# Kernel optimization log

Measured on AMD Instinct MI355X. Metric: run time of the kernel, lower is better.

## Reference

```python
import jax, jax.numpy as jnp
import numpy as np

B, T, D_MODEL, N_HEADS, D_FF = 2, 2048, 512, 8, 2048
D_HEAD = D_MODEL // N_HEADS
EPS_LN = 1e-5
DEN_MIN = 1e-6


def setup_inputs() -> dict:
    key = jax.random.key(0)
    ks = jax.random.split(key, 12)
    def lin_w(k, din, dout):
        return jax.random.normal(k, (din, dout), jnp.float32) / np.sqrt(din).astype(np.float32)
    return {
        "x": jax.random.normal(ks[0], (B, T, D_MODEL), jnp.float32),
        "ln1_g": jnp.ones((D_MODEL,), jnp.float32),
        "ln1_b": jnp.zeros((D_MODEL,), jnp.float32),
        "Wq": lin_w(ks[1], D_MODEL, D_MODEL), "bq": jnp.zeros((D_MODEL,), jnp.float32),
        "Wk": lin_w(ks[2], D_MODEL, D_MODEL), "bk": jnp.zeros((D_MODEL,), jnp.float32),
        "Wv": lin_w(ks[3], D_MODEL, D_MODEL), "bv": jnp.zeros((D_MODEL,), jnp.float32),
        "Wo": lin_w(ks[4], D_MODEL, D_MODEL), "bo": jnp.zeros((D_MODEL,), jnp.float32),
        "ln2_g": jnp.ones((D_MODEL,), jnp.float32),
        "ln2_b": jnp.zeros((D_MODEL,), jnp.float32),
        "W1": lin_w(ks[5], D_MODEL, D_FF), "b1": jnp.zeros((D_FF,), jnp.float32),
        "W2": lin_w(ks[6], D_FF, D_MODEL), "b2": jnp.zeros((D_MODEL,), jnp.float32),
    }


def layer_norm(x, g, b):
    mu = jnp.mean(x, axis=-1, keepdims=True)
    var = jnp.var(x, axis=-1, keepdims=True)
    return (x - mu) * jax.lax.rsqrt(var + EPS_LN) * g + b


def causal_linear_attention(Q, K, V):
    # Q,K,V: (B,H,T,D); feature map already applied to Q,K.
    # Running summary S_t = cumsum_j phi(K_j) outer V_j, shape (B,H,T,D,D)
    KV = jnp.cumsum(K[..., :, None] * V[..., None, :], axis=2)
    z = jnp.cumsum(K, axis=2)                                   # (B,H,T,D)
    num = jnp.einsum('bhtd,bhtdm->bhtm', Q, KV)                 # (B,H,T,D)
    den = jnp.maximum(jnp.einsum('bhtd,bhtd->bht', Q, z), DEN_MIN)[..., None]
    return num / den


def reference(x, ln1_g, ln1_b, Wq, bq, Wk, bk, Wv, bv, Wo, bo,
              ln2_g, ln2_b, W1, b1, W2, b2):
    Bx, Tx, _ = x.shape
    # --- sublayer 1: pre-norm causal linear attention + residual ---
    h = layer_norm(x, ln1_g, ln1_b)
    def heads(y):  # (B,T,D_MODEL) -> (B,H,T,D_HEAD)
        return y.reshape(Bx, Tx, N_HEADS, D_HEAD).transpose(0, 2, 1, 3)
    Q = jax.nn.elu(heads(h @ Wq + bq)) + 1.0
    K = jax.nn.elu(heads(h @ Wk + bk)) + 1.0
    V = heads(h @ Wv + bv)
    attn = causal_linear_attention(Q, K, V)                     # (B,H,T,D)
    attn = attn.transpose(0, 2, 1, 3).reshape(Bx, Tx, D_MODEL)
    x = x + (attn @ Wo + bo)
    # --- sublayer 2: pre-norm FFN + residual (dropout=0, eval mode) ---
    h2 = layer_norm(x, ln2_g, ln2_b)
    ffn = jax.nn.relu(h2 @ W1 + b1) @ W2 + b2
    return x + ffn
```

## Files before the change

### kernel.cpp

```cpp
#include <hip/hip_runtime.h>
#include <hip/hip_bf16.h>
#include <cstdint>

#define T_SEQ   2048
#define DM      512
#define NH      8
#define DH      64
#define BATCH   2
#define MROWS   4096
#define DFF     2048
#define CHUNK   64
#define NCHUNK  32
#define BHN     16
#define ST_STRIDE 4160

typedef __attribute__((ext_vector_type(8))) short bf16x8;
typedef __attribute__((ext_vector_type(4))) float f32x4;
typedef __hip_bfloat16 bf16;

__device__ __forceinline__ void g2lds16(const bf16* g, bf16* l) {
    __builtin_amdgcn_global_load_lds(
        (const __attribute__((address_space(1))) unsigned int*)g,
        (__attribute__((address_space(3))) unsigned int*)l, 16, 0, 0);
}

template<bool INIT>
__global__ __launch_bounds__(128) void ln_kernel(
    const float* __restrict__ x, const float* __restrict__ g,
    const float* __restrict__ b, bf16* __restrict__ y,
    const float* __restrict__ b2, float* __restrict__ oinit)
{
    int row = blockIdx.x;
    int t = threadIdx.x;
    const float4* xr = (const float4*)(x + (size_t)row * DM);
    float4 v = xr[t];
    float s  = v.x + v.y + v.z + v.w;
    float s2 = v.x*v.x + v.y*v.y + v.z*v.z + v.w*v.w;
#pragma unroll
    for (int off = 32; off > 0; off >>= 1) {
        s  += __shfl_down(s,  off);
        s2 += __shfl_down(s2, off);
    }
    __shared__ float sh[4];
    if ((t & 63) == 0) { sh[(t >> 6) * 2] = s; sh[(t >> 6) * 2 + 1] = s2; }
    __syncthreads();
    s  = sh[0] + sh[2];
    s2 = sh[1] + sh[3];
    float mu  = s * (1.0f / DM);
    float var = s2 * (1.0f / DM) - mu * mu;
    float rs  = rsqrtf(var + 1e-5f);
    float4 gg = ((const float4*)g)[t];
    float4 bb = ((const float4*)b)[t];
    union { short4 s4; bf16 h[4]; } u;
    u.h[0] = __float2bfloat16((v.x - mu) * rs * gg.x + bb.x);
    u.h[1] = __float2bfloat16((v.y - mu) * rs * gg.y + bb.y);
    u.h[2] = __float2bfloat16((v.z - mu) * rs * gg.z + bb.z);
    u.h[3] = __float2bfloat16((v.w - mu) * rs * gg.w + bb.w);
    *(short4*)(y + (size_t)row * DM + t * 4) = u.s4;
    if (INIT) {
        float4 b2v = ((const float4*)b2)[t];
        float4 ov = make_float4(v.x + b2v.x, v.y + b2v.y, v.z + b2v.z, v.w + b2v.w);
        ((float4*)(oinit + (size_t)row * DM))[t] = ov;
    }
}

__global__ __launch_bounds__(256) void wcvt_all(
    const float* __restrict__ Wq, const float* __restrict__ Wk,
    const float* __restrict__ Wv, const float* __restrict__ Wo,
    const float* __restrict__ W1, const float* __restrict__ W2,
    bf16* __restrict__ QKVWT, bf16* __restrict__ WoT,
    bf16* __restrict__ W1T, bf16* __restrict__ W2T)
{
    __shared__ float tile[64][65];
    int bid = blockIdx.x;
    const float* src; bf16* dst; int K, N, txi, tyi;
    if (bid < 256) {
        int m = bid >> 6, t = bid & 63;
        src = m == 0 ? Wq : m == 1 ? Wk : m == 2 ? Wv : Wo;
        dst = m == 0 ? QKVWT : m == 1 ? QKVWT + 512*512
            : m == 2 ? QKVWT + 1024*512 : WoT;
        K = 512; N = 512; txi = t & 7; tyi = t >> 3;
    } else if (bid < 512) {
        int t = bid - 256;
        src = W1; dst = W1T; K = 512; N = 2048; txi = t & 31; tyi = t >> 5;
    } else {
        int t = bid - 512;
        src = W2; dst = W2T; K = 2048; N = 512; txi = t & 7; tyi = t >> 3;
    }
    int k0 = tyi * 64, n0 = txi * 64;
    int tid = threadIdx.x;
    int tr = tid >> 4, tc = (tid & 15) * 4;
#pragma unroll
    for (int i = 0; i < 4; i++) {
        float4 v = *(const float4*)(src + (size_t)(k0 + tr + i*16) * N + n0 + tc);
        tile[tr + i*16][tc+0] = v.x; tile[tr + i*16][tc+1] = v.y;
        tile[tr + i*16][tc+2] = v.z; tile[tr + i*16][tc+3] = v.w;
    }
    __syncthreads();
#pragma unroll
    for (int i = 0; i < 4; i++) {
        int n = tr + i*16;
        union { short4 s4; bf16 h[4]; } u;
#pragma unroll
        for (int j = 0; j < 4; j++) u.h[j] = __float2bfloat16(tile[tc+j][n]);
        *(short4*)(dst + (size_t)(n0 + n) * K + k0 + tc) = u.s4;
    }
}

template<int BM, int BN, int WM, int WN, int MODE>
__global__ __launch_bounds__(WM*WN*64) void mfma_gemm(
    const bf16* __restrict__ A, const bf16* __restrict__ Bt,
    const float* __restrict__ bias0, const float* __restrict__ bias1,
    const float* __restrict__ bias2, const float* __restrict__ res,
    float* __restrict__ outF,
    float* __restrict__ outQ, float* __restrict__ outK, float* __restrict__ outV,
    bf16* __restrict__ outB, int M, int N, int K)
{
    constexpr int BK = 64;
    constexpr int WAVES = WM * WN;
    constexpr int WTM = BM / WM, WTN = BN / WN;
    constexpr int FM = WTM / 16, FN = WTN / 16;
    constexpr int IA = BM / 8 / WAVES, IB = BN / 8 / WAVES;
    __shared__ bf16 As[BM * BK];
    __shared__ bf16 Bs[BN * BK];
    const int tid = threadIdx.x;
    const int w = tid >> 6, lane = tid & 63;
    const int wr = w / WN, wc = w % WN;
    const int bm0 = blockIdx.y * BM, bn0 = blockIdx.x * BN;
    const int srow = lane >> 3;
    const int scol = (lane & 7) * 8;

    int kbeg = 0, kend = K;
    if (MODE == 3) { int half = K >> 1; kbeg = blockIdx.z * half; kend = kbeg + half; }

    f32x4 acc[FM][FN];
#pragma unroll
    for (int m = 0; m < FM; m++)
#pragma unroll
        for (int n = 0; n < FN; n++) acc[m][n] = (f32x4){0.f,0.f,0.f,0.f};

    for (int k0 = kbeg; k0 < kend; k0 += BK) {
#pragma unroll
        for (int i = 0; i < IA; i++) {
            int c = i*WAVES + w;
            g2lds16(A + (size_t)(bm0 + c*8 + srow) * K + k0 + scol, &As[c*512]);
        }
#pragma unroll
        for (int i = 0; i < IB; i++) {
            int c = i*WAVES + w;
            g2lds16(Bt + (size_t)(bn0 + c*8 + srow) * K + k0 + scol, &Bs[c*512]);
        }
        __syncthreads();
#pragma unroll
        for (int kk = 0; kk < 2; kk++) {
            bf16x8 af[FM], bfr[FN];
#pragma unroll
            for (int m = 0; m < FM; m++)
                af[m] = *(const bf16x8*)&As[(wr*WTM + m*16 + (lane&15))*BK + kk*32 + (lane>>4)*8];
#pragma unroll
            for (int n = 0; n < FN; n++)
                bfr[n] = *(const bf16x8*)&Bs[(wc*WTN + n*16 + (lane&15))*BK + kk*32 + (lane>>4)*8];
#pragma unroll
            for (int m = 0; m < FM; m++)
#pragma unroll
                for (int n = 0; n < FN; n++)
                    acc[m][n] = __builtin_amdgcn_mfma_f32_16x16x32_bf16(af[m], bfr[n], acc[m][n], 0, 0, 0);
        }
        __syncthreads();
    }

    const int lr = (lane >> 4) * 4;
    const int lc = lane & 15;
#pragma unroll
    for (int m = 0; m < FM; m++) {
#pragma unroll
        for (int n = 0; n < FN; n++) {
            int col = bn0 + wc*WTN + n*16 + lc;
#pragma unroll
            for (int j = 0; j < 4; j++) {
                int r = bm0 + wr*WTM + m*16 + lr + j;
                float v = acc[m][n][j];
                if (MODE == 0) {
                    int which = col >> 9;
                    int cc = col & 511;
                    float bv_ = which == 0 ? bias0[cc] : which == 1 ? bias1[cc] : bias2[cc];
                    v += bv_;
                    if (which < 2) v = v > 0.f ? v + 1.f : __expf(v);
                    int hh = cc >> 6, dd = cc & 63;
                    int bb = r >> 11, tt = r & 2047;
                    float* dst = which == 0 ? outQ : which == 1 ? outK : outV;
                    dst[((((size_t)(bb*NH + hh)) * T_SEQ + tt) << 6) + dd] = v;
                } else if (MODE == 1) {
                    v += bias0[col] + res[(size_t)r * N + col];
                    outF[(size_t)r * N + col] = v;
                } else if (MODE == 2) {
                    v += bias0[col];
                    v = fmaxf(v, 0.f);
                    outB[(size_t)r * N + col] = __float2bfloat16(v);
                } else {
                    unsafeAtomicAdd(&outF[(size_t)r * N + col], v);
                }
            }
        }
    }
}

__global__ __launch_bounds__(256) void attn_chunk_sum(
    const float* __restrict__ Kb, const float* __restrict__ Vb,
    float* __restrict__ St)
{
    int blk = blockIdx.x;
    const float* Kp = Kb + (size_t)blk * (CHUNK * DH);
    const float* Vp = Vb + (size_t)blk * (CHUNK * DH);
    float* Sp = St + (size_t)blk * ST_STRIDE;
    __shared__ float Ks[64][64];
    __shared__ float Vs[64][64];
    int tid = threadIdx.x;
#pragma unroll
    for (int i = 0; i < 4; i++) {
        ((float4*)Ks)[tid + i*256] = ((const float4*)Kp)[tid + i*256];
        ((float4*)Vs)[tid + i*256] = ((const float4*)Vp)[tid + i*256];
    }
    __syncthreads();
    int r  = tid >> 2;
    int c0 = (tid & 3) * 16;
    float s[16];
#pragma unroll
    for (int i = 0; i < 16; i++) s[i] = 0.0f;
    for (int t = 0; t < 64; t++) {
        float kv = Ks[t][r];
        const float4* vr = (const float4*)&Vs[t][c0];
        float4 v0 = vr[0], v1 = vr[1], v2 = vr[2], v3 = vr[3];
        s[0]+=kv*v0.x; s[1]+=kv*v0.y; s[2]+=kv*v0.z; s[3]+=kv*v0.w;
        s[4]+=kv*v1.x; s[5]+=kv*v1.y; s[6]+=kv*v1.z; s[7]+=kv*v1.w;
        s[8]+=kv*v2.x; s[9]+=kv*v2.y; s[10]+=kv*v2.z; s[11]+=kv*v2.w;
        s[12]+=kv*v3.x; s[13]+=kv*v3.y; s[14]+=kv*v3.z; s[15]+=kv*v3.w;
    }
#pragma unroll
    for (int i = 0; i < 4; i++) {
        float4 ov = make_float4(s[i*4+0], s[i*4+1], s[i*4+2], s[i*4+3]);
        *(float4*)(Sp + (size_t)r*64 + c0 + i*4) = ov;
    }
    if (tid < 64) {
        float z = 0.0f;
        for (int t = 0; t < 64; t++) z += Ks[t][tid];
        Sp[4096 + tid] = z;
    }
}

__global__ __launch_bounds__(64) void attn_scan(float* __restrict__ St)
{
    int f4 = blockIdx.x * 64 + threadIdx.x;
    if (f4 >= ST_STRIDE / 4) return;
    int bh = blockIdx.y;
    float4* base = (float4*)(St + (size_t)bh * NCHUNK * ST_STRIDE) + f4;
    float4 run = make_float4(0.f, 0.f, 0.f, 0.f);
#pragma unroll 4
    for (int ch = 0; ch < NCHUNK; ch++) {
        float4* p = base + (size_t)ch * (ST_STRIDE / 4);
        float4 t = *p;
        *p = run;
        run.x += t.x; run.y += t.y; run.z += t.z; run.w += t.w;
    }
}

__global__ __launch_bounds__(256) void attn_out_k(
    const float* __restrict__ Qb, const float* __restrict__ Kb,
    const float* __restrict__ Vb, const float* __restrict__ St,
    bf16* __restrict__ attnb)
{
    int blk = blockIdx.x;
    int bh = blk >> 5, ch = blk & 31;
    int b = bh >> 3, h = bh & 7;
    const float* Qp = Qb + (size_t)blk * 4096;
    const float* Kp = Kb + (size_t)blk * 4096;
    const float* Vp = Vb + (size_t)blk * 4096;
    const float* Sp = St + (size_t)blk * ST_STRIDE;
    __shared__ float Qs[64][68];
    __shared__ float Kt[64][68];
    __shared__ float Vs[64][68];
    __shared__ float Ss[64][68];
    __shared__ float Amat[64][65];
    __shared__ float zs[64];
    int tid = threadIdx.x;
#pragma unroll
    for (int i = 0; i < 4; i++) {
        int fi = tid + i*256;
        int t  = fi >> 4;
        int d4 = (fi & 15) * 4;
        float4 q = ((const float4*)Qp)[fi];
        float4 k = ((const float4*)Kp)[fi];
        float4 v = ((const float4*)Vp)[fi];
        float4 s = ((const float4*)Sp)[fi];
        *(float4*)&Qs[t][d4] = q;
        *(float4*)&Vs[t][d4] = v;
        *(float4*)&Ss[t][d4] = s;
        Kt[d4+0][t] = k.x; Kt[d4+1][t] = k.y; Kt[d4+2][t] = k.z; Kt[d4+3][t] = k.w;
    }
    if (tid < 64) zs[tid] = Sp[4096 + tid];
    __syncthreads();
    int r  = tid >> 2;
    int c0 = (tid & 3) * 16;
    float a[16];
#pragma unroll
    for (int i = 0; i < 16; i++) a[i] = 0.0f;
    for (int d = 0; d < 64; d++) {
        float q = Qs[r][d];
        const float4* kr = (const float4*)&Kt[d][c0];
        float4 k0 = kr[0], k1 = kr[1], k2 = kr[2], k3 = kr[3];
        a[0]+=q*k0.x; a[1]+=q*k0.y; a[2]+=q*k0.z; a[3]+=q*k0.w;
        a[4]+=q*k1.x; a[5]+=q*k1.y; a[6]+=q*k1.z; a[7]+=q*k1.w;
        a[8]+=q*k2.x; a[9]+=q*k2.y; a[10]+=q*k2.z; a[11]+=q*k2.w;
        a[12]+=q*k3.x; a[13]+=q*k3.y; a[14]+=q*k3.z; a[15]+=q*k3.w;
    }
#pragma unroll
    for (int i = 0; i < 16; i++) Amat[r][c0+i] = a[i];
    __syncthreads();
    float den = 0.0f;
    for (int d = 0; d < 64; d++) den += Qs[r][d] * zs[d];
    for (int j = 0; j <= r; j++) den += Amat[r][j];
    den = fmaxf(den, 1e-6f);
    float num[16];
#pragma unroll
    for (int i = 0; i < 16; i++) num[i] = 0.0f;
    for (int d = 0; d < 64; d++) {
        float q = Qs[r][d];
        const float4* sv = (const float4*)&Ss[d][c0];
        float4 s0 = sv[0], s1 = sv[1], s2 = sv[2], s3 = sv[3];
        num[0]+=q*s0.x; num[1]+=q*s0.y; num[2]+=q*s0.z; num[3]+=q*s0.w;
        num[4]+=q*s1.x; num[5]+=q*s1.y; num[6]+=q*s1.z; num[7]+=q*s1.w;
        num[8]+=q*s2.x; num[9]+=q*s2.y; num[10]+=q*s2.z; num[11]+=q*s2.w;
        num[12]+=q*s3.x; num[13]+=q*s3.y; num[14]+=q*s3.z; num[15]+=q*s3.w;
    }
    for (int j = 0; j <= r; j++) {
        float aj = Amat[r][j];
        const float4* vv = (const float4*)&Vs[j][c0];
        float4 v0 = vv[0], v1 = vv[1], v2 = vv[2], v3 = vv[3];
        num[0]+=aj*v0.x; num[1]+=aj*v0.y; num[2]+=aj*v0.z; num[3]+=aj*v0.w;
        num[4]+=aj*v1.x; num[5]+=aj*v1.y; num[6]+=aj*v1.z; num[7]+=aj*v1.w;
        num[8]+=aj*v2.x; num[9]+=aj*v2.y; num[10]+=aj*v2.z; num[11]+=aj*v2.w;
        num[12]+=aj*v3.x; num[13]+=aj*v3.y; num[14]+=aj*v3.z; num[15]+=aj*v3.w;
    }
    float inv = 1.0f / den;
    union { short4 s4[4]; bf16 hh[16]; } u;
#pragma unroll
    for (int i = 0; i < 16; i++) u.hh[i] = __float2bfloat16(num[i] * inv);
    short4* op = (short4*)(attnb + ((size_t)b * T_SEQ + ch*64 + r) * DM + h*64 + c0);
#pragma unroll
    for (int i = 0; i < 4; i++) op[i] = u.s4[i];
}

extern "C" void kernel_launch(void* const* d_in, const int* in_sizes, int n_in,
                              void* d_out, int out_size, void* d_ws, size_t ws_size,
                              hipStream_t stream)
{
    (void)in_sizes; (void)n_in; (void)out_size; (void)ws_size;
    const float* x     = (const float*)d_in[0];
    const float* ln1_g = (const float*)d_in[1];
    const float* ln1_b = (const float*)d_in[2];
    const float* Wq = (const float*)d_in[3];
    const float* bq = (const float*)d_in[4];
    const float* Wk = (const float*)d_in[5];
    const float* bk = (const float*)d_in[6];
    const float* Wv = (const float*)d_in[7];
    const float* bv = (const float*)d_in[8];
    const float* Wo = (const float*)d_in[9];
    const float* bo = (const float*)d_in[10];
    const float* ln2_g = (const float*)d_in[11];
    const float* ln2_b = (const float*)d_in[12];
    const float* W1 = (const float*)d_in[13];
    const float* b1 = (const float*)d_in[14];
    const float* W2 = (const float*)d_in[15];
    const float* b2 = (const float*)d_in[16];
    float* out = (float*)d_out;
    char* base = (char*)d_ws;

    bf16*  h_bf  = (bf16*)(base + 0);
    bf16*  h2_bf = (bf16*)(base + 4194304);
    bf16*  attnb = (bf16*)(base + 8388608);
    bf16*  QKVWT = (bf16*)(base + 12582912);
    bf16*  WoT   = (bf16*)(base + 14155776);
    bf16*  W1T   = (bf16*)(base + 14680064);
    bf16*  W2T   = (bf16*)(base + 16777216);
    float* Qb    = (float*)(base + 18874368);
    float* Kb    = (float*)(base + 27262976);
    float* Vb    = (float*)(base + 35651584);
    float* St    = (float*)(base + 44040192);
    float* X2    = (float*)(base + 52559872);
    bf16*  FF    = (bf16*)(base + 60948480);

    wcvt_all<<<768, 256, 0, stream>>>(Wq, Wk, Wv, Wo, W1, W2,
                                      QKVWT, WoT, W1T, W2T);

    ln_kernel<false><<<MROWS, 128, 0, stream>>>(x, ln1_g, ln1_b, h_bf, nullptr, nullptr);

    mfma_gemm<128,128,4,2,0><<<dim3(12, 32), 512, 0, stream>>>(
        h_bf, QKVWT, bq, bk, bv, nullptr, nullptr, Qb, Kb, Vb, nullptr,
        MROWS, 1536, 512);

    attn_chunk_sum<<<BHN*NCHUNK, 256, 0, stream>>>(Kb, Vb, St);
    attn_scan<<<dim3(17, BHN), 64, 0, stream>>>(St);
    attn_out_k<<<BHN*NCHUNK, 256, 0, stream>>>(Qb, Kb, Vb, St, attnb);

    mfma_gemm<64,64,2,2,1><<<dim3(8, 64), 256, 0, stream>>>(
        attnb, WoT, bo, nullptr, nullptr, x, X2, nullptr, nullptr, nullptr, nullptr,
        MROWS, 512, 512);

    ln_kernel<true><<<MROWS, 128, 0, stream>>>(X2, ln2_g, ln2_b, h2_bf, b2, out);

    mfma_gemm<128,128,4,2,2><<<dim3(16, 32), 512, 0, stream>>>(
        h2_bf, W1T, b1, nullptr, nullptr, nullptr, nullptr, nullptr, nullptr, nullptr, FF,
        MROWS, DFF, 512);

    mfma_gemm<128,64,2,2,3><<<dim3(8, 32, 2), 256, 0, stream>>>(
        FF, W2T, nullptr, nullptr, nullptr, nullptr, out, nullptr, nullptr, nullptr, nullptr,
        MROWS, 512, 2048);
}
```

Before: 228.7 us.

## Store Q/K/V intermediates in bf16, bf16 attention matrix, XCD-aware GEMM block swizzle

The QKV GEMM epilogue now writes Q, K and V as bf16 instead of fp32, and the chunk-sum and chunk-output attention kernels load and widen bf16x8 vectors. This halves the intermediate traffic to and from global memory. The in-chunk attention score matrix is kept in bf16 in shared memory. An XCD-aware block-index swizzle is added to all GEMMs to improve L2 locality across chiplets. The cost is reduced precision in the attention path and extra index arithmetic.

New measurement: 212.6 us. 1.08x faster.

```diff
diff --git a/kernel.cpp b/kernel.cpp
--- a/kernel.cpp
+++ b/kernel.cpp
@@ -22,6 +22,21 @@
     __builtin_amdgcn_global_load_lds(
         (const __attribute__((address_space(1))) unsigned int*)g,
         (__attribute__((address_space(3))) unsigned int*)l, 16, 0, 0);
+}
+
+__device__ __forceinline__ float b2f(short s) {
+    union { unsigned u; float f; } x;
+    x.u = ((unsigned)(unsigned short)s) << 16;
+    return x.f;
+}
+
+__device__ __forceinline__ void xcd_swizzle(int gx, int gy, int& bx, int& by) {
+    int lin = by * gx + bx;
+    int nwg = gx * gy;
+    int q = nwg >> 3, r = nwg & 7;
+    int xcd = lin & 7, loc = lin >> 3;
+    int swz = (xcd < r ? xcd * (q + 1) : r * (q + 1) + (xcd - r) * q) + loc;
+    bx = swz % gx; by = swz / gx;
 }
 
 template<bool INIT>
@@ -113,7 +128,7 @@
     const float* __restrict__ bias0, const float* __restrict__ bias1,
     const float* __restrict__ bias2, const float* __restrict__ res,
     float* __restrict__ outF,
-    float* __restrict__ outQ, float* __restrict__ outK, float* __restrict__ outV,
+    bf16* __restrict__ outQ, bf16* __restrict__ outK, bf16* __restrict__ outV,
     bf16* __restrict__ outB, int M, int N, int K)
 {
     constexpr int BK = 64;
@@ -126,7 +141,9 @@
     const int tid = threadIdx.x;
     const int w = tid >> 6, lane = tid & 63;
     const int wr = w / WN, wc = w % WN;
-    const int bm0 = blockIdx.y * BM, bn0 = blockIdx.x * BN;
+    int bx = blockIdx.x, by = blockIdx.y;
+    xcd_swizzle(gridDim.x, gridDim.y, bx, by);
+    const int bm0 = by * BM, bn0 = bx * BN;
     const int srow = lane >> 3;
     const int scol = (lane & 7) * 8;
 
@@ -188,8 +205,8 @@
                     if (which < 2) v = v > 0.f ? v + 1.f : __expf(v);
                     int hh = cc >> 6, dd = cc & 63;
                     int bb = r >> 11, tt = r & 2047;
-                    float* dst = which == 0 ? outQ : which == 1 ? outK : outV;
-                    dst[((((size_t)(bb*NH + hh)) * T_SEQ + tt) << 6) + dd] = v;
+                    bf16* dst = which == 0 ? outQ : which == 1 ? outK : outV;
+                    dst[((((size_t)(bb*NH + hh)) * T_SEQ + tt) << 6) + dd] = __float2bfloat16(v);
                 } else if (MODE == 1) {
                     v += bias0[col] + res[(size_t)r * N + col];
                     outF[(size_t)r * N + col] = v;
@@ -206,20 +223,27 @@
 }
 
 __global__ __launch_bounds__(256) void attn_chunk_sum(
-    const float* __restrict__ Kb, const float* __restrict__ Vb,
+    const bf16* __restrict__ Kb, const bf16* __restrict__ Vb,
     float* __restrict__ St)
 {
     int blk = blockIdx.x;
-    const float* Kp = Kb + (size_t)blk * (CHUNK * DH);
-    const float* Vp = Vb + (size_t)blk * (CHUNK * DH);
+    const bf16* Kp = Kb + (size_t)blk * (CHUNK * DH);
+    const bf16* Vp = Vb + (size_t)blk * (CHUNK * DH);
     float* Sp = St + (size_t)blk * ST_STRIDE;
     __shared__ float Ks[64][64];
     __shared__ float Vs[64][64];
     int tid = threadIdx.x;
 #pragma unroll
-    for (int i = 0; i < 4; i++) {
-        ((float4*)Ks)[tid + i*256] = ((const float4*)Kp)[tid + i*256];
-        ((float4*)Vs)[tid + i*256] = ((const float4*)Vp)[tid + i*256];
+    for (int i = 0; i < 2; i++) {
+        int idx = tid + i*256;
+        int t = idx >> 3, d8 = (idx & 7) * 8;
+        bf16x8 k8 = ((const bf16x8*)Kp)[idx];
+        bf16x8 v8 = ((const bf16x8*)Vp)[idx];
+#pragma unroll
+        for (int j = 0; j < 8; j++) {
+            Ks[t][d8+j] = b2f(k8[j]);
+            Vs[t][d8+j] = b2f(v8[j]);
+        }
     }
     __syncthreads();
     int r  = tid >> 2;
@@ -265,37 +289,45 @@
 }
 
 __global__ __launch_bounds__(256) void attn_out_k(
-    const float* __restrict__ Qb, const float* __restrict__ Kb,
-    const float* __restrict__ Vb, const float* __restrict__ St,
+    const bf16* __restrict__ Qb, const bf16* __restrict__ Kb,
+    const bf16* __restrict__ Vb, const float* __restrict__ St,
     bf16* __restrict__ attnb)
 {
     int blk = blockIdx.x;
     int bh = blk >> 5, ch = blk & 31;
     int b = bh >> 3, h = bh & 7;
-    const float* Qp = Qb + (size_t)blk * 4096;
-    const float* Kp = Kb + (size_t)blk * 4096;
-    const float* Vp = Vb + (size_t)blk * 4096;
+    const bf16*  Qp = Qb + (size_t)blk * 4096;
+    const bf16*  Kp = Kb + (size_t)blk * 4096;
+    const bf16*  Vp = Vb + (size_t)blk * 4096;
     const float* Sp = St + (size_t)blk * ST_STRIDE;
     __shared__ float Qs[64][68];
     __shared__ float Kt[64][68];
     __shared__ float Vs[64][68];
     __shared__ float Ss[64][68];
-    __shared__ float Amat[64][65];
+    __shared__ bf16  Amat[64][72];
     __shared__ float zs[64];
     int tid = threadIdx.x;
+#pragma unroll
+    for (int i = 0; i < 2; i++) {
+        int idx = tid + i*256;
+        int t = idx >> 3, d8 = (idx & 7) * 8;
+        bf16x8 q8 = ((const bf16x8*)Qp)[idx];
+        bf16x8 k8 = ((const bf16x8*)Kp)[idx];
+        bf16x8 v8 = ((const bf16x8*)Vp)[idx];
+#pragma unroll
+        for (int j = 0; j < 8; j++) {
+            Qs[t][d8+j] = b2f(q8[j]);
+            Vs[t][d8+j] = b2f(v8[j]);
+            Kt[d8+j][t] = b2f(k8[j]);
+        }
+    }
 #pragma unroll
     for (int i = 0; i < 4; i++) {
         int fi = tid + i*256;
         int t  = fi >> 4;
         int d4 = (fi & 15) * 4;
-        float4 q = ((const float4*)Qp)[fi];
-        float4 k = ((const float4*)Kp)[fi];
-        float4 v = ((const float4*)Vp)[fi];
         float4 s = ((const float4*)Sp)[fi];
-        *(float4*)&Qs[t][d4] = q;
-        *(float4*)&Vs[t][d4] = v;
         *(float4*)&Ss[t][d4] = s;
-        Kt[d4+0][t] = k.x; Kt[d4+1][t] = k.y; Kt[d4+2][t] = k.z; Kt[d4+3][t] = k.w;
     }
     if (tid < 64) zs[tid] = Sp[4096 + tid];
     __syncthreads();
@@ -313,12 +345,15 @@
         a[8]+=q*k2.x; a[9]+=q*k2.y; a[10]+=q*k2.z; a[11]+=q*k2.w;
         a[12]+=q*k3.x; a[13]+=q*k3.y; a[14]+=q*k3.z; a[15]+=q*k3.w;
     }
-#pragma unroll
-    for (int i = 0; i < 16; i++) Amat[r][c0+i] = a[i];
+    union { bf16x8 v8[2]; bf16 hh[16]; } ua;
+#pragma unroll
+    for (int i = 0; i < 16; i++) ua.hh[i] = __float2bfloat16(a[i]);
+    *(bf16x8*)&Amat[r][c0]   = ua.v8[0];
+    *(bf16x8*)&Amat[r][c0+8] = ua.v8[1];
     __syncthreads();
     float den = 0.0f;
     for (int d = 0; d < 64; d++) den += Qs[r][d] * zs[d];
-    for (int j = 0; j <= r; j++) den += Amat[r][j];
+    for (int j = 0; j <= r; j++) den += b2f(*(const short*)&Amat[r][j]);
     den = fmaxf(den, 1e-6f);
     float num[16];
 #pragma unroll
@@ -333,7 +368,7 @@
         num[12]+=q*s3.x; num[13]+=q*s3.y; num[14]+=q*s3.z; num[15]+=q*s3.w;
     }
     for (int j = 0; j <= r; j++) {
-        float aj = Amat[r][j];
+        float aj = b2f(*(const short*)&Amat[r][j]);
         const float4* vv = (const float4*)&Vs[j][c0];
         float4 v0 = vv[0], v1 = vv[1], v2 = vv[2], v3 = vv[3];
         num[0]+=aj*v0.x; num[1]+=aj*v0.y; num[2]+=aj*v0.z; num[3]+=aj*v0.w;
@@ -374,20 +409,21 @@
     const float* b2 = (const float*)d_in[16];
     float* out = (float*)d_out;
     char* base = (char*)d_ws;
+    const size_t MB = 1048576;
 
     bf16*  h_bf  = (bf16*)(base + 0);
-    bf16*  h2_bf = (bf16*)(base + 4194304);
-    bf16*  attnb = (bf16*)(base + 8388608);
-    bf16*  QKVWT = (bf16*)(base + 12582912);
-    bf16*  WoT   = (bf16*)(base + 14155776);
-    bf16*  W1T   = (bf16*)(base + 14680064);
-    bf16*  W2T   = (bf16*)(base + 16777216);
-    float* Qb    = (float*)(base + 18874368);
-    float* Kb    = (float*)(base + 27262976);
-    float* Vb    = (float*)(base + 35651584);
-    float* St    = (float*)(base + 44040192);
-    float* X2    = (float*)(base + 52559872);
-    bf16*  FF    = (bf16*)(base + 60948480);
+    bf16*  h2_bf = (bf16*)(base + 4*MB);
+    bf16*  attnb = (bf16*)(base + 8*MB);
+    bf16*  QKVWT = (bf16*)(base + 12*MB);
+    bf16*  WoT   = (bf16*)(base + 14*MB);
+    bf16*  W1T   = (bf16*)(base + 15*MB);
+    bf16*  W2T   = (bf16*)(base + 17*MB);
+    bf16*  Qb    = (bf16*)(base + 20*MB);
+    bf16*  Kb    = (bf16*)(base + 24*MB);
+    bf16*  Vb    = (bf16*)(base + 28*MB);
+    float* St    = (float*)(base + 32*MB);
+    float* X2    = (float*)(base + 41*MB);
+    bf16*  FF    = (bf16*)(base + 50*MB);
 
     wcvt_all<<<768, 256, 0, stream>>>(Wq, Wk, Wv, Wo, W1, W2,
                                       QKVWT, WoT, W1T, W2T);
```
